# Optimization experiments

Measured on AMD Instinct MI355X. Metric: run time of the kernel, lower is better.

Reference implementation:

```python
import jax, jax.numpy as jnp
import numpy as np

# --- quantization helpers (I-BERT-style symmetric quantization) ---

def _quant_int(x, scale, bit):
    # round(x/scale) clamped to signed `bit`-bit range (SymmetricQuantFunction)
    n = 2 ** (bit - 1) - 1
    return jnp.clip(jnp.round(x / scale), -n - 1, n)


def quant_linear(x, s_x, W, b, weight_bit=8):
    """QuantLinear: per-output-channel symmetric 8-bit weight quant, int GEMM, dequant.
    Returns (output, bias_scaling_factor[out_features])."""
    n = 2 ** (weight_bit - 1) - 1
    w_scale = jnp.maximum(jnp.max(jnp.abs(W), axis=1), 1e-8) / n          # (out,)
    w_int = _quant_int(W, w_scale[:, None], weight_bit)                   # int-valued (out,in)
    b_scale = w_scale * s_x                                               # (out,) broadcasts with scalar s_x
    b_int = jnp.round(b / b_scale)                                        # 32-bit bias, no clamp needed
    x_int = x / s_x                                                       # int-valued activations
    out_int = jnp.einsum('bsi,oi->bso', x_int, w_int) + b_int
    return out_int * b_scale, b_scale


def quant_act(x, bit):
    """QuantAct: per-tensor symmetric requantization to `bit` bits (dynamic min/max)."""
    n = 2 ** (bit - 1) - 1
    scale = jnp.maximum(jnp.max(jnp.abs(x)), 1e-8) / n                    # scalar
    x_int = _quant_int(x, scale, bit)
    return x_int * scale, scale


def int_gelu(x, s):
    """IntGELU (I-BERT): integer 2nd-order polynomial approximation of erf."""
    k = 1.4142
    c0, c1 = -0.2888, -1.769
    c2 = 1.0 / c0
    SHIFT = 14  # 'const' in the original code

    x_int = x / s
    se = s / k  # scaling factor fed to int_erf
    # --- int_erf ---
    b_int = jnp.floor(c1 / se)
    c_int = jnp.floor(c2 / se ** 2)
    sign = jnp.sign(x_int)
    abs_int = jnp.minimum(jnp.abs(x_int), -b_int)
    y_int = sign * ((abs_int + b_int) ** 2 + c_int)
    se2 = se ** 2 * c0
    y_int = jnp.floor(y_int / 2 ** SHIFT)
    se2 = se2 * 2 ** SHIFT
    # --- gelu = x * (erf/2 + 1/2) in integer form ---
    shift_int = jnp.floor(1.0 / se2)
    out_int = x_int * (y_int + shift_int)
    s_out = s * se2 / 2
    return out_int * s_out, s_out


def setup_inputs() -> dict:
    key = jax.random.key(0)
    k_x, k_w1, k_b1, k_w2, k_b2 = jax.random.split(key, 5)
    B, S, D, H = 8, 1024, 768, 3072
    x = jax.random.normal(k_x, (B, S, D), dtype=jnp.float32)
    act_scaling_factor = jnp.full((1,), 0.02, dtype=jnp.float32)
    # pre-quantize x onto its input grid (x arrives already quantized in the real pipeline)
    x = jnp.round(x / act_scaling_factor) * act_scaling_factor
    W1 = jax.random.normal(k_w1, (H, D), dtype=jnp.float32) * 0.02
    b1 = jax.random.normal(k_b1, (H,), dtype=jnp.float32) * 0.02
    W2 = jax.random.normal(k_w2, (D, H), dtype=jnp.float32) * 0.02
    b2 = jax.random.normal(k_b2, (D,), dtype=jnp.float32) * 0.02
    return {"x": x, "act_scaling_factor": act_scaling_factor,
            "W1": W1, "b1": b1, "W2": W2, "b2": b2}


def reference(x, act_scaling_factor, W1, b1, W2, b2):
    s = act_scaling_factor
    h, s = quant_linear(x, s, W1, b1)       # fc1: int8 GEMM + dequant
    h, s = quant_act(h, 8)                  # qact_gelu
    h, s = int_gelu(h, s)                   # IntGELU
    h, s = quant_act(h, 8)                  # qact1 (drop=0.0 -> identity)
    h, s = quant_linear(h, s, W2, b2)       # fc2
    h, s = quant_act(h, 16)                 # qact2 (16-bit)
    return h, s
```

## Files before the change

kernel.cpp:

```cpp
#include <hip/hip_runtime.h>

typedef _Float16 half8  __attribute__((ext_vector_type(8)));
typedef _Float16 half4v __attribute__((ext_vector_type(4)));
typedef float f32x4 __attribute__((ext_vector_type(4)));
typedef int int4v __attribute__((ext_vector_type(4)));

#define M_DIM 8192
#define D_DIM 768
#define H_DIM 3072

#define WS_WSCALE2   16
#define WS_BINT1     (WS_WSCALE2 + 768*4)
#define WS_BSCALE1   (WS_BINT1 + 3072*4)
#define WS_BINT2     (WS_BSCALE1 + 3072*4)
#define WS_BSCALE2   (WS_BINT2 + 768*4)
#define WS_XQ        34560UL
#define WS_WQ1       (WS_XQ  + (size_t)M_DIM*D_DIM*2)
#define WS_WQ2I      (WS_WQ1 + (size_t)H_DIM*D_DIM*2)
#define WS_H1        (WS_WQ2I + (size_t)D_DIM*H_DIM)
#define WS_Q2        WS_H1
#define WS_H2        (WS_H1 + (size_t)M_DIM*H_DIM)
#define WS_Q1        (WS_H1 + (size_t)M_DIM*H_DIM*4)

__device__ __forceinline__ void gl_lds16(const _Float16* g, _Float16* l) {
  __builtin_amdgcn_global_load_lds(
      (const __attribute__((address_space(1))) void*)g,
      (__attribute__((address_space(3))) void*)l, 16, 0, 0);
}
__device__ __forceinline__ void gl_lds16c(const char* g, char* l) {
  __builtin_amdgcn_global_load_lds(
      (const __attribute__((address_space(1))) void*)g,
      (__attribute__((address_space(3))) void*)l, 16, 0, 0);
}

struct GeluP { float scale1, bintg, cintg, shiftint, s_out; };

__device__ __forceinline__ GeluP gelu_params(float max1) {
  GeluP p;
  p.scale1 = fmaxf(max1, 1e-8f) / 127.0f;
  float se = p.scale1 / 1.4142f;
  p.bintg = floorf(-1.769f / se);
  p.cintg = floorf(((float)(1.0 / -0.2888)) / (se * se));
  float se2 = ((se * se) * -0.2888f) * 16384.0f;
  p.shiftint = floorf(1.0f / se2);
  p.s_out = (p.scale1 * se2) * 0.5f;
  return p;
}

__device__ __forceinline__ float gelu_val(const GeluP& p, float qf) {
  float sg = (qf > 0.f) ? 1.f : ((qf < 0.f) ? -1.f : 0.f);
  float aq = fminf(fabsf(qf), -p.bintg);
  float t = aq + p.bintg;
  float y = sg * (t * t + p.cintg);
  float yf = floorf(y * (1.0f / 16384.0f));
  return (qf * (yf + p.shiftint)) * p.s_out;
}

__global__ __launch_bounds__(256)
void k1_prep(const float* __restrict__ W1, const float* __restrict__ b1,
             const float* __restrict__ W2, const float* __restrict__ sxp,
             _Float16* __restrict__ wq1, char* __restrict__ wq2i,
             float* __restrict__ wscale2, float* __restrict__ bint1,
             float* __restrict__ bscale1, unsigned* __restrict__ wsu)
{
  if (blockIdx.x == 0 && threadIdx.x == 0) { wsu[0] = 0u; wsu[1] = 0u; wsu[2] = 0u; }
  int w = blockIdx.x * 4 + (threadIdx.x >> 6);
  int lane = threadIdx.x & 63;
  if (w < H_DIM) {
    const float* row = W1 + (size_t)w * D_DIM;
    f32x4 v[3]; float m = 0.f;
#pragma unroll
    for (int t = 0; t < 3; t++) {
      v[t] = *(const f32x4*)(row + t * 256 + lane * 4);
#pragma unroll
      for (int j = 0; j < 4; j++) m = fmaxf(m, fabsf(v[t][j]));
    }
#pragma unroll
    for (int off = 32; off >= 1; off >>= 1) m = fmaxf(m, __shfl_xor(m, off));
    float wsc = fmaxf(m, 1e-8f) / 127.0f;
    _Float16* orow = wq1 + (size_t)w * D_DIM;
#pragma unroll
    for (int t = 0; t < 3; t++) {
      half4v h;
#pragma unroll
      for (int j = 0; j < 4; j++) {
        float q = fminf(fmaxf(rintf(v[t][j] / wsc), -128.f), 127.f);
        h[j] = (_Float16)q;
      }
      *(half4v*)(orow + t * 256 + lane * 4) = h;
    }
    if (lane == 0) {
      float bs = wsc * sxp[0];
      bint1[w] = rintf(b1[w] / bs);
      bscale1[w] = bs;
    }
  } else {
    int o = w - H_DIM;
    const float* row = W2 + (size_t)o * H_DIM;
    f32x4 v[12]; float m = 0.f;
#pragma unroll
    for (int t = 0; t < 12; t++) {
      v[t] = *(const f32x4*)(row + t * 256 + lane * 4);
#pragma unroll
      for (int j = 0; j < 4; j++) m = fmaxf(m, fabsf(v[t][j]));
    }
#pragma unroll
    for (int off = 32; off >= 1; off >>= 1) m = fmaxf(m, __shfl_xor(m, off));
    float wsc = fmaxf(m, 1e-8f) / 127.0f;
    unsigned* orow = (unsigned*)(wq2i + (size_t)o * H_DIM);
#pragma unroll
    for (int t = 0; t < 12; t++) {
      unsigned pk = 0;
#pragma unroll
      for (int j = 0; j < 4; j++) {
        float q = fminf(fmaxf(rintf(v[t][j] / wsc), -128.f), 127.f);
        pk |= ((unsigned)(unsigned char)(char)(int)q) << (8 * j);
      }
      orow[t * 64 + lane] = pk;
    }
    if (lane == 0) wscale2[o] = wsc;
  }
}

__global__ __launch_bounds__(256)
void k2_quant_x(const float* __restrict__ x, const float* __restrict__ sxp,
                _Float16* __restrict__ xq, int n4)
{
  float sx = sxp[0];
  int stride = gridDim.x * blockDim.x;
  for (int i = blockIdx.x * blockDim.x + threadIdx.x; i < n4; i += stride) {
    f32x4 v = ((const f32x4*)x)[i];
    half4v h;
#pragma unroll
    for (int j = 0; j < 4; j++) h[j] = (_Float16)(v[j] / sx);
    ((half4v*)xq)[i] = h;
  }
}

__global__ __launch_bounds__(256)
void gemm_f16(const _Float16* __restrict__ A, const _Float16* __restrict__ B,
              const float* __restrict__ bint, const float* __restrict__ bscale,
              float* __restrict__ C, unsigned* __restrict__ maxw, int N, int K)
{
  __shared__ _Float16 sA[2][128 * 32];
  __shared__ _Float16 sB[2][128 * 32];
  __shared__ float wred[4];
  const int tid = threadIdx.x;
  const int wid = tid >> 6;
  const int lane = tid & 63;
  const int m0 = blockIdx.x * 128;
  const int n0 = blockIdx.y * 128;
  const int wr = (wid >> 1) * 64;
  const int wc = (wid & 1) * 64;
  const int lrow = lane & 15;
  const int lk = (lane >> 4) * 8;
  const int srow = lane >> 2;
  const int schunk = (lane & 3) * 8;

  const _Float16* Ab = A + (size_t)m0 * K;
  const _Float16* Bb = B + (size_t)n0 * K;

  f32x4 acc[4][4];
#pragma unroll
  for (int i = 0; i < 4; i++)
#pragma unroll
    for (int j = 0; j < 4; j++) acc[i][j] = (f32x4){0.f, 0.f, 0.f, 0.f};

  const int nt = K / 32;

#define STAGE_F16(bufi, k0) do {                                              \
    _Float16* dA = sA[bufi]; _Float16* dB = sB[bufi];                         \
    _Pragma("unroll")                                                         \
    for (int r = 0; r < 2; r++) {                                             \
      const int rq = r * 4 + wid;                                             \
      const int row = rq * 16 + srow;                                         \
      gl_lds16(Ab + (size_t)row * K + ((k0) + schunk), dA + rq * 512);        \
      gl_lds16(Bb + (size_t)row * K + ((k0) + schunk), dB + rq * 512);        \
    } } while (0)

  STAGE_F16(0, 0);
  __syncthreads();
  int cur = 0;
  for (int t = 0; t < nt; ++t) {
    if (t + 1 < nt) STAGE_F16(cur ^ 1, (t + 1) * 32);
    half8 a[4], b[4];
#pragma unroll
    for (int f = 0; f < 4; f++) {
      a[f] = *(const half8*)&sA[cur][(wr + f * 16 + lrow) * 32 + lk];
      b[f] = *(const half8*)&sB[cur][(wc + f * 16 + lrow) * 32 + lk];
    }
#pragma unroll
    for (int i = 0; i < 4; i++)
#pragma unroll
      for (int j = 0; j < 4; j++)
        acc[i][j] = __builtin_amdgcn_mfma_f32_16x16x32_f16(a[i], b[j], acc[i][j], 0, 0, 0);
    __syncthreads();
    cur ^= 1;
  }
#undef STAGE_F16

  float tmax = 0.f;
  const int orow0 = m0 + wr + (lane >> 4) * 4;
  const int ocol0 = n0 + wc + lrow;
#pragma unroll
  for (int j = 0; j < 4; j++) {
    const int col = ocol0 + j * 16;
    const float bi = bint[col];
    const float bs = bscale[col];
#pragma unroll
    for (int i = 0; i < 4; i++) {
#pragma unroll
      for (int e = 0; e < 4; e++) {
        const int rowm = orow0 + i * 16 + e;
        float v = (acc[i][j][e] + bi) * bs;
        C[(size_t)rowm * N + col] = v;
        tmax = fmaxf(tmax, fabsf(v));
      }
    }
  }
#pragma unroll
  for (int off = 32; off >= 1; off >>= 1) tmax = fmaxf(tmax, __shfl_xor(tmax, off));
  if (lane == 0) wred[wid] = tmax;
  __syncthreads();
  if (tid == 0) {
    float bm = fmaxf(fmaxf(wred[0], wred[1]), fmaxf(wred[2], wred[3]));
    atomicMax(maxw, __float_as_uint(bm));
  }
}

__global__ __launch_bounds__(256)
void k4_gelu(const float* __restrict__ h1, const unsigned* __restrict__ wsu,
             char* __restrict__ q1, unsigned* __restrict__ maxw, int n4)
{
  GeluP p = gelu_params(__uint_as_float(wsu[0]));
  float tmax = 0.f;
  int stride = gridDim.x * blockDim.x;
  for (int i = blockIdx.x * blockDim.x + threadIdx.x; i < n4; i += stride) {
    f32x4 h = ((const f32x4*)h1)[i];
    unsigned pack = 0;
#pragma unroll
    for (int j = 0; j < 4; j++) {
      float qf = fminf(fmaxf(rintf(h[j] / p.scale1), -128.f), 127.f);
      tmax = fmaxf(tmax, fabsf(gelu_val(p, qf)));
      pack |= ((unsigned)(unsigned char)(char)(int)qf) << (8 * j);
    }
    ((unsigned*)q1)[i] = pack;
  }
#pragma unroll
  for (int off = 32; off >= 1; off >>= 1) tmax = fmaxf(tmax, __shfl_xor(tmax, off));
  __shared__ float wred[4];
  int wid = threadIdx.x >> 6;
  if ((threadIdx.x & 63) == 0) wred[wid] = tmax;
  __syncthreads();
  if (threadIdx.x == 0) {
    float bm = fmaxf(fmaxf(wred[0], wred[1]), fmaxf(wred[2], wred[3]));
    atomicMax(maxw, __float_as_uint(bm));
  }
}

__global__ __launch_bounds__(256)
void k6_bias(const unsigned* __restrict__ wsu, const float* __restrict__ wscale2,
             const float* __restrict__ b2, float* __restrict__ bint2,
             float* __restrict__ bscale2)
{
  float scale2 = fmaxf(__uint_as_float(wsu[1]), 1e-8f) / 127.0f;
  for (int o = threadIdx.x; o < D_DIM; o += 256) {
    float bs = wscale2[o] * scale2;
    bint2[o] = rintf(b2[o] / bs);
    bscale2[o] = bs;
  }
}

__global__ __launch_bounds__(256)
void k5_q2(const char* __restrict__ q1, const unsigned* __restrict__ wsu,
           char* __restrict__ q2, int n16)
{
  GeluP p = gelu_params(__uint_as_float(wsu[0]));
  float scale2 = fmaxf(__uint_as_float(wsu[1]), 1e-8f) / 127.0f;
  int stride = gridDim.x * blockDim.x;
  for (int i = blockIdx.x * blockDim.x + threadIdx.x; i < n16; i += stride) {
    uint4 pk = ((const uint4*)q1)[i];
    uint4 o;
    unsigned* pw[4] = {&o.x, &o.y, &o.z, &o.w};
    unsigned pr[4] = {pk.x, pk.y, pk.z, pk.w};
#pragma unroll
    for (int w = 0; w < 4; w++) {
      unsigned acc = 0;
#pragma unroll
      for (int j = 0; j < 4; j++) {
        float qf = (float)(int)(signed char)(pr[w] >> (8 * j));
        float g = gelu_val(p, qf);
        float q2f = fminf(fmaxf(rintf(g / scale2), -128.f), 127.f);
        acc |= ((unsigned)(unsigned char)(char)(int)q2f) << (8 * j);
      }
      *pw[w] = acc;
    }
    ((uint4*)q2)[i] = o;
  }
}

__global__ __launch_bounds__(256)
void gemm_i8(const char* __restrict__ A, const char* __restrict__ B,
             const float* __restrict__ bint, const float* __restrict__ bscale,
             float* __restrict__ C, unsigned* __restrict__ maxw, int N, int K)
{
  __shared__ char sA[2][64 * 64];
  __shared__ char sB[2][128 * 64];
  __shared__ float wred[4];
  const int tid = threadIdx.x;
  const int wid = tid >> 6;
  const int lane = tid & 63;
  const int m0 = blockIdx.x * 64;
  const int n0 = blockIdx.y * 128;
  const int wr = (wid >> 1) * 32;
  const int wc = (wid & 1) * 64;
  const int lrow = lane & 15;
  const int lkc = (lane >> 4) * 16;
  const int srow = lane >> 2;
  const int schunk = (lane & 3) * 16;

  const char* Ab = A + (size_t)m0 * K;
  const char* Bb = B + (size_t)n0 * K;

  int4v acc[2][4];
#pragma unroll
  for (int i = 0; i < 2; i++)
#pragma unroll
    for (int j = 0; j < 4; j++) acc[i][j] = (int4v){0, 0, 0, 0};

  const int nt = K / 64;

#define STAGE_I8(bufi, k0) do {                                               \
    char* dA = sA[bufi]; char* dB = sB[bufi];                                 \
    gl_lds16c(Ab + (size_t)(wid * 16 + srow) * K + ((k0) + schunk),           \
              dA + wid * 1024);                                               \
    _Pragma("unroll")                                                         \
    for (int r = 0; r < 2; r++) {                                             \
      const int rq = r * 4 + wid;                                             \
      gl_lds16c(Bb + (size_t)(rq * 16 + srow) * K + ((k0) + schunk),          \
                dB + rq * 1024);                                              \
    } } while (0)

  STAGE_I8(0, 0);
  __syncthreads();
  int cur = 0;
  for (int t = 0; t < nt; ++t) {
    if (t + 1 < nt) STAGE_I8(cur ^ 1, (t + 1) * 64);
    int4v a[2], b[4];
#pragma unroll
    for (int f = 0; f < 2; f++)
      a[f] = *(const int4v*)&sA[cur][(wr + f * 16 + lrow) * 64 + lkc];
#pragma unroll
    for (int f = 0; f < 4; f++)
      b[f] = *(const int4v*)&sB[cur][(wc + f * 16 + lrow) * 64 + lkc];
#pragma unroll
    for (int i = 0; i < 2; i++)
#pragma unroll
      for (int j = 0; j < 4; j++)
        acc[i][j] = __builtin_amdgcn_mfma_i32_16x16x64_i8(a[i], b[j], acc[i][j], 0, 0, 0);
    __syncthreads();
    cur ^= 1;
  }
#undef STAGE_I8

  float tmax = 0.f;
  const int orow0 = m0 + wr + (lane >> 4) * 4;
  const int ocol0 = n0 + wc + lrow;
#pragma unroll
  for (int j = 0; j < 4; j++) {
    const int col = ocol0 + j * 16;
    const float bi = bint[col];
    const float bs = bscale[col];
#pragma unroll
    for (int i = 0; i < 2; i++) {
#pragma unroll
      for (int e = 0; e < 4; e++) {
        const int rowm = orow0 + i * 16 + e;
        float v = ((float)acc[i][j][e] + bi) * bs;
        C[(size_t)rowm * N + col] = v;
        tmax = fmaxf(tmax, fabsf(v));
      }
    }
  }
#pragma unroll
  for (int off = 32; off >= 1; off >>= 1) tmax = fmaxf(tmax, __shfl_xor(tmax, off));
  if (lane == 0) wred[wid] = tmax;
  __syncthreads();
  if (tid == 0) {
    float bm = fmaxf(fmaxf(wred[0], wred[1]), fmaxf(wred[2], wred[3]));
    atomicMax(maxw, __float_as_uint(bm));
  }
}

__global__ __launch_bounds__(256)
void k7_final(const float* __restrict__ h2, const unsigned* __restrict__ wsu,
              float* __restrict__ out, int n4, int ntot)
{
  float scale16 = fmaxf(__uint_as_float(wsu[2]), 1e-8f) / 32767.0f;
  int stride = gridDim.x * blockDim.x;
  for (int i = blockIdx.x * blockDim.x + threadIdx.x; i < n4; i += stride) {
    f32x4 v = ((const f32x4*)h2)[i];
    f32x4 o;
#pragma unroll
    for (int j = 0; j < 4; j++) {
      float q = fminf(fmaxf(rintf(v[j] / scale16), -32768.f), 32767.f);
      o[j] = q * scale16;
    }
    ((f32x4*)out)[i] = o;
  }
  if (blockIdx.x == 0 && threadIdx.x == 0) out[ntot] = scale16;
}

extern "C" void kernel_launch(void* const* d_in, const int* in_sizes, int n_in,
                              void* d_out, int out_size, void* d_ws, size_t ws_size,
                              hipStream_t stream)
{
  (void)in_sizes; (void)n_in; (void)out_size; (void)ws_size;
  const float* x  = (const float*)d_in[0];
  const float* sx = (const float*)d_in[1];
  const float* W1 = (const float*)d_in[2];
  const float* b1 = (const float*)d_in[3];
  const float* W2 = (const float*)d_in[4];
  const float* b2 = (const float*)d_in[5];
  float* out = (float*)d_out;
  char* ws = (char*)d_ws;

  unsigned* wsu   = (unsigned*)ws;
  float* wscale2  = (float*)(ws + WS_WSCALE2);
  float* bint1    = (float*)(ws + WS_BINT1);
  float* bscale1  = (float*)(ws + WS_BSCALE1);
  float* bint2    = (float*)(ws + WS_BINT2);
  float* bscale2  = (float*)(ws + WS_BSCALE2);
  _Float16* xq    = (_Float16*)(ws + WS_XQ);
  _Float16* wq1   = (_Float16*)(ws + WS_WQ1);
  char* wq2i      = (char*)(ws + WS_WQ2I);
  float* h1       = (float*)(ws + WS_H1);
  char* q2        = (char*)(ws + WS_Q2);
  float* h2       = (float*)(ws + WS_H2);
  char* q1        = (char*)(ws + WS_Q1);

  k1_prep<<<dim3(960), dim3(256), 0, stream>>>(W1, b1, W2, sx, wq1, wq2i, wscale2, bint1, bscale1, wsu);
  k2_quant_x<<<dim3(2048), dim3(256), 0, stream>>>(x, sx, xq, (M_DIM * D_DIM) / 4);
  gemm_f16<<<dim3(64, 24), dim3(256), 0, stream>>>(xq, wq1, bint1, bscale1, h1, wsu + 0, H_DIM, D_DIM);
  k4_gelu<<<dim3(2048), dim3(256), 0, stream>>>(h1, wsu, q1, wsu + 1, (M_DIM * H_DIM) / 4);
  k6_bias<<<dim3(1), dim3(256), 0, stream>>>(wsu, wscale2, b2, bint2, bscale2);
  k5_q2<<<dim3(2048), dim3(256), 0, stream>>>(q1, wsu, q2, (M_DIM * H_DIM) / 16);
  gemm_i8<<<dim3(128, 6), dim3(256), 0, stream>>>(q2, wq2i, bint2, bscale2, h2, wsu + 2, D_DIM, H_DIM);
  k7_final<<<dim3(2048), dim3(256), 0, stream>>>(h2, wsu, out, (M_DIM * D_DIM) / 4, M_DIM * D_DIM);
}
```

Before: 195.9 us.

## Rewrite fc1 GEMM with 128x256 tiles, 3-stage LDS pipeline and swizzle

Replaces the fc1 fp16 GEMM with a 512-thread kernel that computes 128x256 output tiles, so each A tile is reused across twice as many columns. Global-to-LDS loads now use a three-slot ring with explicit vmcnt waits and a single barrier per k-step, keeping two tiles in flight instead of one. LDS rows are XOR-swizzled to cut bank conflicts, and the MFMA block runs at raised wave priority. In exchange the kernel uses more LDS and registers per block and launches half as many blocks, which may lower occupancy.

After: 186.8 us. 1.05x faster.

```diff
diff --git a/kernel.cpp b/kernel.cpp
--- a/kernel.cpp
+++ b/kernel.cpp
@@ -137,28 +137,54 @@
   }
 }
 
-__global__ __launch_bounds__(256)
-void gemm_f16(const _Float16* __restrict__ A, const _Float16* __restrict__ B,
-              const float* __restrict__ bint, const float* __restrict__ bscale,
-              float* __restrict__ C, unsigned* __restrict__ maxw, int N, int K)
-{
-  __shared__ _Float16 sA[2][128 * 32];
-  __shared__ _Float16 sB[2][128 * 32];
-  __shared__ float wred[4];
+#define SLOT_A 4096
+#define SLOT_B 8192
+#define SLOT_SZ (SLOT_A + SLOT_B)
+
+__global__ __launch_bounds__(512)
+void gemm_f16_dp(const _Float16* __restrict__ A, const _Float16* __restrict__ B,
+                 const float* __restrict__ bint, const float* __restrict__ bscale,
+                 float* __restrict__ C, unsigned* __restrict__ maxw, int N, int K)
+{
+  __shared__ _Float16 lds[3 * SLOT_SZ];
+  __shared__ float wred[8];
   const int tid = threadIdx.x;
   const int wid = tid >> 6;
   const int lane = tid & 63;
   const int m0 = blockIdx.x * 128;
-  const int n0 = blockIdx.y * 128;
-  const int wr = (wid >> 1) * 64;
-  const int wc = (wid & 1) * 64;
-  const int lrow = lane & 15;
-  const int lk = (lane >> 4) * 8;
-  const int srow = lane >> 2;
-  const int schunk = (lane & 3) * 8;
-
-  const _Float16* Ab = A + (size_t)m0 * K;
-  const _Float16* Bb = B + (size_t)n0 * K;
+  const int n0 = blockIdx.y * 256;
+  const int wm = wid >> 2;
+  const int wn = wid & 3;
+
+  const int sr = lane >> 2;
+  const int sc = lane & 3;
+  const int ra  = wid * 16 + sr;
+  const int csa = sc ^ ((ra >> 1) & 3);
+  const int rb  = wid * 16 + sr;
+  const int csb = sc ^ ((rb >> 1) & 3);
+  const _Float16* pa  = A + (size_t)(m0 + ra) * K + csa * 8;
+  const _Float16* pb0 = B + (size_t)(n0 + rb) * K + csb * 8;
+  const _Float16* pb1 = B + (size_t)(n0 + rb + 128) * K + csb * 8;
+  _Float16* const da  = lds;
+  _Float16* const db0 = lds + SLOT_A;
+  _Float16* const db1 = lds + SLOT_A + 4096;
+
+#define STAGE_DP(t, s) do {                                                  \
+    const int _o = (s) * SLOT_SZ + wid * 512;                                \
+    gl_lds16(pa  + (size_t)(t) * 32, da  + _o);                              \
+    gl_lds16(pb0 + (size_t)(t) * 32, db0 + _o);                              \
+    gl_lds16(pb1 + (size_t)(t) * 32, db1 + _o);                              \
+  } while (0)
+
+  int aoff[4], boff[4];
+  const int ks = lane >> 4;
+#pragma unroll
+  for (int f = 0; f < 4; f++) {
+    int r = wm * 64 + f * 16 + (lane & 15);
+    aoff[f] = r * 64 + ((ks ^ ((r >> 1) & 3)) * 16);
+    int rn = wn * 64 + f * 16 + (lane & 15);
+    boff[f] = SLOT_A * 2 + rn * 64 + ((ks ^ ((rn >> 1) & 3)) * 16);
+  }
 
   f32x4 acc[4][4];
 #pragma unroll
@@ -167,41 +193,35 @@
     for (int j = 0; j < 4; j++) acc[i][j] = (f32x4){0.f, 0.f, 0.f, 0.f};
 
   const int nt = K / 32;
-
-#define STAGE_F16(bufi, k0) do {                                              \
-    _Float16* dA = sA[bufi]; _Float16* dB = sB[bufi];                         \
-    _Pragma("unroll")                                                         \
-    for (int r = 0; r < 2; r++) {                                             \
-      const int rq = r * 4 + wid;                                             \
-      const int row = rq * 16 + srow;                                         \
-      gl_lds16(Ab + (size_t)row * K + ((k0) + schunk), dA + rq * 512);        \
-      gl_lds16(Bb + (size_t)row * K + ((k0) + schunk), dB + rq * 512);        \
-    } } while (0)
-
-  STAGE_F16(0, 0);
-  __syncthreads();
-  int cur = 0;
+  STAGE_DP(0, 0);
+  STAGE_DP(1, 1);
   for (int t = 0; t < nt; ++t) {
-    if (t + 1 < nt) STAGE_F16(cur ^ 1, (t + 1) * 32);
+    const int s = t % 3;
+    if (t + 1 < nt) asm volatile("s_waitcnt vmcnt(3)" ::: "memory");
+    else            asm volatile("s_waitcnt vmcnt(0)" ::: "memory");
+    __builtin_amdgcn_s_barrier();
+    if (t + 2 < nt) STAGE_DP(t + 2, (t + 2) % 3);
+    const char* sb = (const char*)(lds + s * SLOT_SZ);
     half8 a[4], b[4];
 #pragma unroll
-    for (int f = 0; f < 4; f++) {
-      a[f] = *(const half8*)&sA[cur][(wr + f * 16 + lrow) * 32 + lk];
-      b[f] = *(const half8*)&sB[cur][(wc + f * 16 + lrow) * 32 + lk];
-    }
+    for (int f = 0; f < 4; f++) a[f] = *(const half8*)(sb + aoff[f]);
+#pragma unroll
+    for (int f = 0; f < 4; f++) b[f] = *(const half8*)(sb + boff[f]);
+    asm volatile("s_waitcnt lgkmcnt(0)" ::: "memory");
+    __builtin_amdgcn_sched_barrier(0);
+    __builtin_amdgcn_s_setprio(1);
 #pragma unroll
     for (int i = 0; i < 4; i++)
 #pragma unroll
       for (int j = 0; j < 4; j++)
         acc[i][j] = __builtin_amdgcn_mfma_f32_16x16x32_f16(a[i], b[j], acc[i][j], 0, 0, 0);
-    __syncthreads();
-    cur ^= 1;
-  }
-#undef STAGE_F16
+    __builtin_amdgcn_s_setprio(0);
+  }
+#undef STAGE_DP
 
   float tmax = 0.f;
-  const int orow0 = m0 + wr + (lane >> 4) * 4;
-  const int ocol0 = n0 + wc + lrow;
+  const int orow0 = m0 + wm * 64 + (lane >> 4) * 4;
+  const int ocol0 = n0 + wn * 64 + (lane & 15);
 #pragma unroll
   for (int j = 0; j < 4; j++) {
     const int col = ocol0 + j * 16;
@@ -223,7 +243,9 @@
   if (lane == 0) wred[wid] = tmax;
   __syncthreads();
   if (tid == 0) {
-    float bm = fmaxf(fmaxf(wred[0], wred[1]), fmaxf(wred[2], wred[3]));
+    float bm = 0.f;
+#pragma unroll
+    for (int i = 0; i < 8; i++) bm = fmaxf(bm, wred[i]);
     atomicMax(maxw, __float_as_uint(bm));
   }
 }
@@ -441,7 +463,7 @@
 
   k1_prep<<<dim3(960), dim3(256), 0, stream>>>(W1, b1, W2, sx, wq1, wq2i, wscale2, bint1, bscale1, wsu);
   k2_quant_x<<<dim3(2048), dim3(256), 0, stream>>>(x, sx, xq, (M_DIM * D_DIM) / 4);
-  gemm_f16<<<dim3(64, 24), dim3(256), 0, stream>>>(xq, wq1, bint1, bscale1, h1, wsu + 0, H_DIM, D_DIM);
+  gemm_f16_dp<<<dim3(64, 12), dim3(512), 0, stream>>>(xq, wq1, bint1, bscale1, h1, wsu + 0, H_DIM, D_DIM);
   k4_gelu<<<dim3(2048), dim3(256), 0, stream>>>(h1, wsu, q1, wsu + 1, (M_DIM * H_DIM) / 4);
   k6_bias<<<dim3(1), dim3(256), 0, stream>>>(wsu, wscale2, b2, bint2, bscale2);
   k5_q2<<<dim3(2048), dim3(256), 0, stream>>>(q1, wsu, q2, (M_DIM * H_DIM) / 16);
```
